# Optimization experiments

Hardware: AMD Instinct MI355X
Metric: run time of the kernel (lower is better)

## Reference

```python
import jax, jax.numpy as jnp
import numpy as np

C = 64
CQ = C // 8


def setup_inputs() -> dict:
    key = jax.random.key(0)
    ks = jax.random.split(key, 8)
    x = jax.random.normal(ks[0], (8, C, 64, 64), dtype=jnp.float32)
    s = 1.0 / np.sqrt(C)
    Wq = jax.random.normal(ks[1], (CQ, C), dtype=jnp.float32) * s
    bq = jax.random.normal(ks[2], (CQ,), dtype=jnp.float32) * s
    Wk = jax.random.normal(ks[3], (CQ, C), dtype=jnp.float32) * s
    bk = jax.random.normal(ks[4], (CQ,), dtype=jnp.float32) * s
    Wv = jax.random.normal(ks[5], (C, C), dtype=jnp.float32) * s
    bv = jax.random.normal(ks[6], (C,), dtype=jnp.float32) * s
    gamma = jnp.array([0.5], dtype=jnp.float32)  # nonzero so value path contributes
    return {"x": x, "Wq": Wq, "bq": bq, "Wk": Wk, "bk": bk, "Wv": Wv, "bv": bv, "gamma": gamma}


def reference(x, Wq, bq, Wk, bk, Wv, bv, gamma):
    B, Cc, H, W = x.shape
    xf = x.reshape(B, Cc, H * W)  # [B, C, N]
    # 1x1 conv == channel-mixing linear
    f = jnp.einsum('oc,bcn->bon', Wq, xf) + bq[None, :, None]  # [B, C/8, N]
    g = jnp.einsum('oc,bcn->bon', Wk, xf) + bk[None, :, None]  # [B, C/8, N]
    h = jnp.einsum('oc,bcn->bon', Wv, xf) + bv[None, :, None]  # [B, C, N]
    # scores[b,i,j] = f[b,:,i] . g[b,:,j]; softmax over dim=1 (query dim i)
    scores = jnp.einsum('bdi,bdj->bij', f, g)  # [B, N, N]
    beta = jax.nn.softmax(scores, axis=1)
    o = gamma[0] * jnp.einsum('bcn,bnm->bcm', h, beta) + xf
    return o.reshape(B, Cc, H, W)
```

## Files before the change

kernel.cpp:

```cpp
#include <hip/hip_runtime.h>
#include <hip/hip_fp16.h>


typedef _Float16 half8_t __attribute__((ext_vector_type(8)));
typedef _Float16 half4_t __attribute__((ext_vector_type(4)));
typedef _Float16 half2_t __attribute__((ext_vector_type(2)));
typedef __fp16  fp16x2  __attribute__((ext_vector_type(2)));
typedef float float4_t __attribute__((ext_vector_type(4)));

#define NTOK 4096
#define PRH 72
#define LOG2E 1.44269504088896340736f

#if __has_builtin(__builtin_amdgcn_exp2f)
__device__ __forceinline__ float fexp2(float x) { return __builtin_amdgcn_exp2f(x); }
#else
__device__ __forceinline__ float fexp2(float x) { return exp2f(x); }
#endif

__device__ __forceinline__ half2_t pkcvt(float a, float b) {
    fp16x2 v = __builtin_amdgcn_cvt_pkrtz(a, b);
    return __builtin_bit_cast(half2_t, v);
}

__global__ __launch_bounds__(320) void proj_kernel(
    const float* __restrict__ x,
    const float* __restrict__ Wq, const float* __restrict__ bq,
    const float* __restrict__ Wk, const float* __restrict__ bk,
    const float* __restrict__ Wv, const float* __restrict__ bv,
    __half* __restrict__ fTR, __half* __restrict__ gT16, __half* __restrict__ hM)
{
    __shared__ __align__(16) _Float16 xh[32 * PRH];
    const int t      = threadIdx.x;
    const int blk    = blockIdx.x;
    const int b      = blockIdx.y;
    const int n0     = blk * 32;
    const int kt64   = blk >> 1;
    const int t4base = (blk & 1) * 2;

    if (t < 256) {
#pragma unroll
        for (int i = 0; i < 2; i++) {
            const int idx = t + i * 256;
            const int c = idx >> 3, f4 = idx & 7;
            float4 v = *(const float4*)(x + (((size_t)(b * 64 + c)) << 12) + n0 + f4 * 4);
            const int cs = c ^ ((f4 & 3) << 4);
            xh[(f4 * 4 + 0) * PRH + cs] = (_Float16)v.x;
            xh[(f4 * 4 + 1) * PRH + cs] = (_Float16)v.y;
            xh[(f4 * 4 + 2) * PRH + cs] = (_Float16)v.z;
            xh[(f4 * 4 + 3) * PRH + cs] = (_Float16)v.w;
        }
    }

    const int w    = t >> 6;
    const int lane = t & 63;
    const int q    = lane >> 4;
    const int ml   = lane & 15;

    const float* wrow;
    if (w == 0) wrow = (ml < 8) ? (Wq + ml * 64) : (Wk + (ml - 8) * 64);
    else        wrow = Wv + ((w - 1) * 16 + ml) * 64;
    half4_t afr[4];
#pragma unroll
    for (int ks = 0; ks < 4; ks++) {
        float4 wv4 = *(const float4*)(wrow + ks * 16 + q * 4);
        afr[ks] = (half4_t){(_Float16)wv4.x, (_Float16)wv4.y,
                            (_Float16)wv4.z, (_Float16)wv4.w};
    }
    float4 bias4;
    if (w == 0) bias4 = (q < 2) ? *(const float4*)(bq + q * 4)
                                : *(const float4*)(bk + (q - 2) * 4);
    else        bias4 = *(const float4*)(bv + (w - 1) * 16 + q * 4);

    __syncthreads();

#pragma unroll
    for (int cg = 0; cg < 2; cg++) {
        const int tok  = cg * 16 + ml;
        const int swz  = (tok >> 2) & 3;
        float4_t acc = (float4_t){0.f, 0.f, 0.f, 0.f};
#pragma unroll
        for (int ks = 0; ks < 4; ks++) {
            half4_t bfr = *(const half4_t*)(&xh[tok * PRH + ((ks ^ swz) * 16 + q * 4)]);
            acc = __builtin_amdgcn_mfma_f32_16x16x16f16(afr[ks], bfr, acc, 0, 0, 0);
        }
        acc[0] += bias4.x; acc[1] += bias4.y; acc[2] += bias4.z; acc[3] += bias4.w;
        const int gtok = n0 + tok;
        const int t4   = t4base + cg;

        if (w == 0) {
            __half* rec = fTR + ((size_t)b << 16) + (size_t)(kt64 * 16 + ml) * 64;
            if (q < 2) {
                half4_t fv = {(_Float16)(acc[0] * LOG2E), (_Float16)(acc[1] * LOG2E),
                              (_Float16)(acc[2] * LOG2E), (_Float16)(acc[3] * LOG2E)};
                *(half4_t*)(rec + q * 16 + t4 * 4) = fv;
            } else {
                half4_t cv = (half4_t){};
                if (q == 2) cv[0] = (_Float16)1.0f;
                *(half4_t*)(rec + q * 16 + t4 * 4) = cv;
            }
            float gn2p = acc[0] * acc[0] + acc[1] * acc[1] +
                         acc[2] * acc[2] + acc[3] * acc[3];
            float gn2 = gn2p + __shfl_xor(gn2p, 16, 64);
            if (q >= 2) {
                half4_t gv = {(_Float16)acc[0], (_Float16)acc[1],
                              (_Float16)acc[2], (_Float16)acc[3]};
                __half* gp = gT16 + (size_t)((b << 12) + gtok) * 16;
                *(half4_t*)(gp + (q - 2) * 4) = gv;
                if (q == 2) {
                    const float M = (LOG2E * 4.6f) * __builtin_sqrtf(gn2) + 1.0f;
                    *(half4_t*)(gp + 8) = (half4_t){(_Float16)(-M), 0, 0, 0};
                } else {
                    *(half4_t*)(gp + 12) = (half4_t){};
                }
            }
        } else {
            const int ch = (w - 1) * 16 + q * 4;
#pragma unroll
            for (int r = 0; r < 4; r++)
                hM[(((size_t)b * 64 + ch + r) << 12) + gtok] = __float2half(acc[r]);
        }
    }
}

template<int NT>
__global__ __launch_bounds__(256) void attn_kernel(
    const __half* __restrict__ fTR, const __half* __restrict__ gT16,
    const __half* __restrict__ hM,
    __half* __restrict__ Pacc, float* __restrict__ Lsum)
{
    __shared__ __align__(16) _Float16 hl[2][64 * PRH];
    const int tid   = threadIdx.x;
    const int w     = tid >> 6;
    const int lane  = tid & 63;
    const int q     = lane >> 4;
    const int ml    = lane & 15;
    const int b     = blockIdx.y;
    const int split = blockIdx.z;
    const int colA  = blockIdx.x * 128 + w * 16 + ml;
    const int colB  = colA + 64;

    half4_t gfA = *(const half4_t*)(gT16 + ((size_t)((b << 12) + colA)) * 16 + q * 4);
    half4_t gfB = *(const half4_t*)(gT16 + ((size_t)((b << 12) + colB)) * 16 + q * 4);

    float4_t accA[4], accB[4];
#pragma unroll
    for (int cg = 0; cg < 4; cg++) {
        accA[cg] = (float4_t){0.f, 0.f, 0.f, 0.f};
        accB[cg] = (float4_t){0.f, 0.f, 0.f, 0.f};
    }
    float4_t accLA = (float4_t){0.f, 0.f, 0.f, 0.f};
    float4_t accLB = (float4_t){0.f, 0.f, 0.f, 0.f};
    const half4_t onesf = {(_Float16)1.0f, (_Float16)1.0f,
                           (_Float16)1.0f, (_Float16)1.0f};

    const int kt0 = split * NT;
    const int c0  = tid >> 3;
    const int g0  = tid & 7;

    const __half* srow0 = hM + ((size_t)(b * 64 + c0) << 12) + kt0 * 64 + g0 * 8;
    const __half* srow1 = srow0 + ((size_t)32 << 12);
    const __half* fptr  = fTR + ((size_t)b << 16) + (size_t)(kt0 * 16 + ml) * 64 + q * 16;

    uint4 s0 = *(const uint4*)srow0;
    uint4 s1 = *(const uint4*)srow1;
    half8_t f01 = *(const half8_t*)fptr;
    half8_t f23 = *(const half8_t*)(fptr + 8);
    *(uint4*)(&hl[0][c0 * PRH + g0 * 8])        = s0;
    *(uint4*)(&hl[0][(c0 + 32) * PRH + g0 * 8]) = s1;
    __syncthreads();

#pragma unroll 1
    for (int kt = 0; kt < NT; kt++) {
        const _Float16* hbL = &hl[kt & 1][ml * PRH + q * 4];
        half4_t afn0 = __builtin_shufflevector(f01, f01, 0, 1, 2, 3);
        half4_t afn1 = __builtin_shufflevector(f01, f01, 4, 5, 6, 7);
        half4_t afn2 = __builtin_shufflevector(f23, f23, 0, 1, 2, 3);
        half4_t afn3 = __builtin_shufflevector(f23, f23, 4, 5, 6, 7);

        float4_t stA0 = __builtin_amdgcn_mfma_f32_16x16x16f16(
            afn0, gfA, (float4_t){0.f, 0.f, 0.f, 0.f}, 0, 0, 0);
        float4_t stA1 = __builtin_amdgcn_mfma_f32_16x16x16f16(
            afn1, gfA, (float4_t){0.f, 0.f, 0.f, 0.f}, 0, 0, 0);
        float4_t stA2 = __builtin_amdgcn_mfma_f32_16x16x16f16(
            afn2, gfA, (float4_t){0.f, 0.f, 0.f, 0.f}, 0, 0, 0);
        float4_t stA3 = __builtin_amdgcn_mfma_f32_16x16x16f16(
            afn3, gfA, (float4_t){0.f, 0.f, 0.f, 0.f}, 0, 0, 0);
        float4_t stB0 = __builtin_amdgcn_mfma_f32_16x16x16f16(
            afn0, gfB, (float4_t){0.f, 0.f, 0.f, 0.f}, 0, 0, 0);
        float4_t stB1 = __builtin_amdgcn_mfma_f32_16x16x16f16(
            afn1, gfB, (float4_t){0.f, 0.f, 0.f, 0.f}, 0, 0, 0);
        float4_t stB2 = __builtin_amdgcn_mfma_f32_16x16x16f16(
            afn2, gfB, (float4_t){0.f, 0.f, 0.f, 0.f}, 0, 0, 0);
        float4_t stB3 = __builtin_amdgcn_mfma_f32_16x16x16f16(
            afn3, gfB, (float4_t){0.f, 0.f, 0.f, 0.f}, 0, 0, 0);

        if (kt + 1 < NT) {
            f01 = *(const half8_t*)(fptr + 1024);
            f23 = *(const half8_t*)(fptr + 1032);
            s0 = *(const uint4*)(srow0 + 64);
            s1 = *(const uint4*)(srow1 + 64);
            fptr  += 1024;
            srow0 += 64;
            srow1 += 64;
        }

        {
            float pA0 = fexp2(stA0[0]), pA1 = fexp2(stA0[1]),
                  pA2 = fexp2(stA0[2]), pA3 = fexp2(stA0[3]);
            float pB0 = fexp2(stB0[0]), pB1 = fexp2(stB0[1]),
                  pB2 = fexp2(stB0[2]), pB3 = fexp2(stB0[3]);
            half2_t a_lo = pkcvt(pA0, pA1), a_hi = pkcvt(pA2, pA3);
            half2_t b_lo = pkcvt(pB0, pB1), b_hi = pkcvt(pB2, pB3);
            half4_t pfA = {a_lo[0], a_lo[1], a_hi[0], a_hi[1]};
            half4_t pfB = {b_lo[0], b_lo[1], b_hi[0], b_hi[1]};
            accLA = __builtin_amdgcn_mfma_f32_16x16x16f16(onesf, pfA, accLA, 0, 0, 0);
            accLB = __builtin_amdgcn_mfma_f32_16x16x16f16(onesf, pfB, accLB, 0, 0, 0);
#pragma unroll
            for (int cg = 0; cg < 4; cg++) {
                half4_t ah = *(const half4_t*)(hbL + cg * (16 * PRH) + 0 * 16);
                accA[cg] = __builtin_amdgcn_mfma_f32_16x16x16f16(ah, pfA, accA[cg], 0, 0, 0);
                accB[cg] = __builtin_amdgcn_mfma_f32_16x16x16f16(ah, pfB, accB[cg], 0, 0, 0);
            }
        }
        {
            float pA0 = fexp2(stA1[0]), pA1 = fexp2(stA1[1]),
                  pA2 = fexp2(stA1[2]), pA3 = fexp2(stA1[3]);
            float pB0 = fexp2(stB1[0]), pB1 = fexp2(stB1[1]),
                  pB2 = fexp2(stB1[2]), pB3 = fexp2(stB1[3]);
            half2_t a_lo = pkcvt(pA0, pA1), a_hi = pkcvt(pA2, pA3);
            half2_t b_lo = pkcvt(pB0, pB1), b_hi = pkcvt(pB2, pB3);
            half4_t pfA = {a_lo[0], a_lo[1], a_hi[0], a_hi[1]};
            half4_t pfB = {b_lo[0], b_lo[1], b_hi[0], b_hi[1]};
            accLA = __builtin_amdgcn_mfma_f32_16x16x16f16(onesf, pfA, accLA, 0, 0, 0);
            accLB = __builtin_amdgcn_mfma_f32_16x16x16f16(onesf, pfB, accLB, 0, 0, 0);
#pragma unroll
            for (int cg = 0; cg < 4; cg++) {
                half4_t ah = *(const half4_t*)(hbL + cg * (16 * PRH) + 1 * 16);
                accA[cg] = __builtin_amdgcn_mfma_f32_16x16x16f16(ah, pfA, accA[cg], 0, 0, 0);
                accB[cg] = __builtin_amdgcn_mfma_f32_16x16x16f16(ah, pfB, accB[cg], 0, 0, 0);
            }
        }
        {
            float pA0 = fexp2(stA2[0]), pA1 = fexp2(stA2[1]),
                  pA2 = fexp2(stA2[2]), pA3 = fexp2(stA2[3]);
            float pB0 = fexp2(stB2[0]), pB1 = fexp2(stB2[1]),
                  pB2 = fexp2(stB2[2]), pB3 = fexp2(stB2[3]);
            half2_t a_lo = pkcvt(pA0, pA1), a_hi = pkcvt(pA2, pA3);
            half2_t b_lo = pkcvt(pB0, pB1), b_hi = pkcvt(pB2, pB3);
            half4_t pfA = {a_lo[0], a_lo[1], a_hi[0], a_hi[1]};
            half4_t pfB = {b_lo[0], b_lo[1], b_hi[0], b_hi[1]};
            accLA = __builtin_amdgcn_mfma_f32_16x16x16f16(onesf, pfA, accLA, 0, 0, 0);
            accLB = __builtin_amdgcn_mfma_f32_16x16x16f16(onesf, pfB, accLB, 0, 0, 0);
#pragma unroll
            for (int cg = 0; cg < 4; cg++) {
                half4_t ah = *(const half4_t*)(hbL + cg * (16 * PRH) + 2 * 16);
                accA[cg] = __builtin_amdgcn_mfma_f32_16x16x16f16(ah, pfA, accA[cg], 0, 0, 0);
                accB[cg] = __builtin_amdgcn_mfma_f32_16x16x16f16(ah, pfB, accB[cg], 0, 0, 0);
            }
        }
        {
            float pA0 = fexp2(stA3[0]), pA1 = fexp2(stA3[1]),
                  pA2 = fexp2(stA3[2]), pA3 = fexp2(stA3[3]);
            float pB0 = fexp2(stB3[0]), pB1 = fexp2(stB3[1]),
                  pB2 = fexp2(stB3[2]), pB3 = fexp2(stB3[3]);
            half2_t a_lo = pkcvt(pA0, pA1), a_hi = pkcvt(pA2, pA3);
            half2_t b_lo = pkcvt(pB0, pB1), b_hi = pkcvt(pB2, pB3);
            half4_t pfA = {a_lo[0], a_lo[1], a_hi[0], a_hi[1]};
            half4_t pfB = {b_lo[0], b_lo[1], b_hi[0], b_hi[1]};
            accLA = __builtin_amdgcn_mfma_f32_16x16x16f16(onesf, pfA, accLA, 0, 0, 0);
            accLB = __builtin_amdgcn_mfma_f32_16x16x16f16(onesf, pfB, accLB, 0, 0, 0);
#pragma unroll
            for (int cg = 0; cg < 4; cg++) {
                half4_t ah = *(const half4_t*)(hbL + cg * (16 * PRH) + 3 * 16);
                accA[cg] = __builtin_amdgcn_mfma_f32_16x16x16f16(ah, pfA, accA[cg], 0, 0, 0);
                accB[cg] = __builtin_amdgcn_mfma_f32_16x16x16f16(ah, pfB, accB[cg], 0, 0, 0);
            }
        }

        if (kt + 1 < NT) {
            _Float16* hn = &hl[(kt + 1) & 1][0];
            *(uint4*)(&hn[c0 * PRH + g0 * 8])        = s0;
            *(uint4*)(&hn[(c0 + 32) * PRH + g0 * 8]) = s1;
        }
        __syncthreads();
    }

    __half* pa = Pacc + (((size_t)(split * 8 + b) * 64) << 12);
#pragma unroll
    for (int cg = 0; cg < 4; cg++)
#pragma unroll
        for (int r = 0; r < 4; r++) {
            int ch = cg * 16 + q * 4 + r;
            pa[((size_t)ch << 12) + colA] = __float2half(accA[cg][r]);
            pa[((size_t)ch << 12) + colB] = __float2half(accB[cg][r]);
        }
    if (q == 0) {
        Lsum[((size_t)(split * 8 + b) << 12) + colA] = accLA[0];
        Lsum[((size_t)(split * 8 + b) << 12) + colB] = accLB[0];
    }
}

template<int S>
__global__ __launch_bounds__(256) void merge_kernel(
    const __half* __restrict__ Pacc, const float* __restrict__ Lsum,
    const float* __restrict__ x, const float* __restrict__ gammap,
    float* __restrict__ out)
{
    __shared__ float invL[64];
    const int tid  = threadIdx.x;
    const int c4   = tid & 15;
    const int chh  = tid >> 4;
    const int b    = blockIdx.y;
    const int col0 = blockIdx.x * 64;
    const int ch   = blockIdx.z * 16 + chh;

    if (tid < 64) {
        float L = 0.f;
#pragma unroll
        for (int s = 0; s < S; s++)
            L += Lsum[((size_t)(s * 8 + b) << 12) + col0 + tid];
        invL[tid] = gammap[0] / L;
    }
    __syncthreads();

    const int cc = c4 * 4;
    const size_t base = (((size_t)b * 64 + ch) << 12) + col0 + cc;
    float4 xv = *(const float4*)(x + base);
    float o0 = 0.f, o1 = 0.f, o2 = 0.f, o3 = 0.f;
#pragma unroll
    for (int s = 0; s < S; s++) {
        half4_t pv = *(const half4_t*)(Pacc +
            (((size_t)(s * 8 + b) * 64 + ch) << 12) + col0 + cc);
        o0 += (float)pv[0];
        o1 += (float)pv[1];
        o2 += (float)pv[2];
        o3 += (float)pv[3];
    }
    float4 ov;
    ov.x = o0 * invL[cc]     + xv.x;
    ov.y = o1 * invL[cc + 1] + xv.y;
    ov.z = o2 * invL[cc + 2] + xv.z;
    ov.w = o3 * invL[cc + 3] + xv.w;
    *(float4*)(out + base) = ov;
}

extern "C" void kernel_launch(void* const* d_in, const int* in_sizes, int n_in,
                              void* d_out, int out_size, void* d_ws, size_t ws_size,
                              hipStream_t stream) {
    const float* x     = (const float*)d_in[0];
    const float* Wq    = (const float*)d_in[1];
    const float* bq    = (const float*)d_in[2];
    const float* Wk    = (const float*)d_in[3];
    const float* bk    = (const float*)d_in[4];
    const float* Wv    = (const float*)d_in[5];
    const float* bv    = (const float*)d_in[6];
    const float* gamma = (const float*)d_in[7];
    float* out = (float*)d_out;

    const size_t fr_bytes  = (size_t)8 * 65536 * 2;
    const size_t g_bytes   = (size_t)8 * NTOK * 16 * 2;
    const size_t hM_bytes  = (size_t)8 * 64 * NTOK * 2;
    const size_t pa_split  = (size_t)8 * 64 * NTOK * 2;
    const size_t l_split   = (size_t)8 * NTOK * sizeof(float);
    const size_t base_need = fr_bytes + g_bytes + hM_bytes;

    int S = 1;
    if (ws_size >= base_need + 4 * (pa_split + l_split)) S = 4;
    else if (ws_size >= base_need + 2 * (pa_split + l_split)) S = 2;

    char* p = (char*)d_ws;
    __half* fTR  = (__half*)p;  p += fr_bytes;
    __half* gT16 = (__half*)p;  p += g_bytes;
    __half* hM   = (__half*)p;  p += hM_bytes;
    __half* Pacc = (__half*)p;  p += (size_t)S * pa_split;
    float*  Lsum = (float*)p;

    proj_kernel<<<dim3(128, 8), 320, 0, stream>>>(x, Wq, bq, Wk, bk, Wv, bv,
                                                  fTR, gT16, hM);
    if (S == 4) {
        attn_kernel<16><<<dim3(32, 8, 4), 256, 0, stream>>>(fTR, gT16, hM, Pacc, Lsum);
        merge_kernel<4><<<dim3(64, 8, 4), 256, 0, stream>>>(Pacc, Lsum, x, gamma, out);
    } else if (S == 2) {
        attn_kernel<32><<<dim3(32, 8, 2), 256, 0, stream>>>(fTR, gT16, hM, Pacc, Lsum);
        merge_kernel<2><<<dim3(64, 8, 4), 256, 0, stream>>>(Pacc, Lsum, x, gamma, out);
    } else {
        attn_kernel<64><<<dim3(32, 8, 1), 256, 0, stream>>>(fTR, gT16, hM, Pacc, Lsum);
        merge_kernel<1><<<dim3(64, 8, 4), 256, 0, stream>>>(Pacc, Lsum, x, gamma, out);
    }
}
```

Baseline: 122.7 us.

## Use 16x16x32 MFMA for PV, add setprio, and allow 8-way key split

Merges pairs of key sub-blocks so the probability-times-value products and row-sum accumulations use the K=32 MFMA instruction, halving the number of MFMA issues in the inner loop. It also raises wave priority around the MFMA blocks with s_setprio. It adds an 8-way split over the key dimension when workspace allows, giving 2048 blocks instead of 1024 to fill the CUs better. The cost is a larger partial buffer and more work in the merge kernel. The new split also depends on how big the workspace is.

Measured after the change: 123.0 us. About the same (+0.2%).

```diff
diff --git a/kernel.cpp b/kernel.cpp
--- a/kernel.cpp
+++ b/kernel.cpp
@@ -123,6 +123,39 @@
     }
 }
 
+#define PAIR(SEA, SOA, SEB, SOB, OFF)                                           \
+    {                                                                           \
+        float eA0 = fexp2(SEA[0]), eA1 = fexp2(SEA[1]),                         \
+              eA2 = fexp2(SEA[2]), eA3 = fexp2(SEA[3]);                         \
+        float oA0 = fexp2(SOA[0]), oA1 = fexp2(SOA[1]),                         \
+              oA2 = fexp2(SOA[2]), oA3 = fexp2(SOA[3]);                         \
+        float eB0 = fexp2(SEB[0]), eB1 = fexp2(SEB[1]),                         \
+              eB2 = fexp2(SEB[2]), eB3 = fexp2(SEB[3]);                         \
+        float oB0 = fexp2(SOB[0]), oB1 = fexp2(SOB[1]),                         \
+              oB2 = fexp2(SOB[2]), oB3 = fexp2(SOB[3]);                         \
+        half2_t eaA = pkcvt(eA0, eA1), ebA = pkcvt(eA2, eA3);                   \
+        half2_t oaA = pkcvt(oA0, oA1), obA = pkcvt(oA2, oA3);                   \
+        half2_t eaB = pkcvt(eB0, eB1), ebB = pkcvt(eB2, eB3);                   \
+        half2_t oaB = pkcvt(oB0, oB1), obB = pkcvt(oB2, oB3);                   \
+        half8_t pA8 = {eaA[0], eaA[1], ebA[0], ebA[1],                          \
+                       oaA[0], oaA[1], obA[0], obA[1]};                         \
+        half8_t pB8 = {eaB[0], eaB[1], ebB[0], ebB[1],                          \
+                       oaB[0], oaB[1], obB[0], obB[1]};                         \
+        __builtin_amdgcn_s_setprio(1);                                          \
+        accLA = __builtin_amdgcn_mfma_f32_16x16x32_f16(ones8, pA8, accLA, 0, 0, 0); \
+        accLB = __builtin_amdgcn_mfma_f32_16x16x32_f16(ones8, pB8, accLB, 0, 0, 0); \
+        _Pragma("unroll")                                                       \
+        for (int cg = 0; cg < 4; cg++) {                                        \
+            half4_t ahE = *(const half4_t*)(hbL + cg * (16 * PRH) + (OFF));     \
+            half4_t ahO = *(const half4_t*)(hbL + cg * (16 * PRH) + (OFF) + 16);\
+            half8_t ah8 = {ahE[0], ahE[1], ahE[2], ahE[3],                      \
+                           ahO[0], ahO[1], ahO[2], ahO[3]};                     \
+            accA[cg] = __builtin_amdgcn_mfma_f32_16x16x32_f16(ah8, pA8, accA[cg], 0, 0, 0); \
+            accB[cg] = __builtin_amdgcn_mfma_f32_16x16x32_f16(ah8, pB8, accB[cg], 0, 0, 0); \
+        }                                                                       \
+        __builtin_amdgcn_s_setprio(0);                                          \
+    }
+
 template<int NT>
 __global__ __launch_bounds__(256) void attn_kernel(
     const __half* __restrict__ fTR, const __half* __restrict__ gT16,
@@ -151,7 +184,8 @@
     }
     float4_t accLA = (float4_t){0.f, 0.f, 0.f, 0.f};
     float4_t accLB = (float4_t){0.f, 0.f, 0.f, 0.f};
-    const half4_t onesf = {(_Float16)1.0f, (_Float16)1.0f,
+    const half8_t ones8 = {(_Float16)1.0f, (_Float16)1.0f, (_Float16)1.0f,
+                           (_Float16)1.0f, (_Float16)1.0f, (_Float16)1.0f,
                            (_Float16)1.0f, (_Float16)1.0f};
 
     const int kt0 = split * NT;
@@ -178,6 +212,7 @@
         half4_t afn2 = __builtin_shufflevector(f23, f23, 0, 1, 2, 3);
         half4_t afn3 = __builtin_shufflevector(f23, f23, 4, 5, 6, 7);
 
+        __builtin_amdgcn_s_setprio(1);
         float4_t stA0 = __builtin_amdgcn_mfma_f32_16x16x16f16(
             afn0, gfA, (float4_t){0.f, 0.f, 0.f, 0.f}, 0, 0, 0);
         float4_t stA1 = __builtin_amdgcn_mfma_f32_16x16x16f16(
@@ -194,6 +229,7 @@
             afn2, gfB, (float4_t){0.f, 0.f, 0.f, 0.f}, 0, 0, 0);
         float4_t stB3 = __builtin_amdgcn_mfma_f32_16x16x16f16(
             afn3, gfB, (float4_t){0.f, 0.f, 0.f, 0.f}, 0, 0, 0);
+        __builtin_amdgcn_s_setprio(0);
 
         if (kt + 1 < NT) {
             f01 = *(const half8_t*)(fptr + 1024);
@@ -205,78 +241,8 @@
             srow1 += 64;
         }
 
-        {
-            float pA0 = fexp2(stA0[0]), pA1 = fexp2(stA0[1]),
-                  pA2 = fexp2(stA0[2]), pA3 = fexp2(stA0[3]);
-            float pB0 = fexp2(stB0[0]), pB1 = fexp2(stB0[1]),
-                  pB2 = fexp2(stB0[2]), pB3 = fexp2(stB0[3]);
-            half2_t a_lo = pkcvt(pA0, pA1), a_hi = pkcvt(pA2, pA3);
-            half2_t b_lo = pkcvt(pB0, pB1), b_hi = pkcvt(pB2, pB3);
-            half4_t pfA = {a_lo[0], a_lo[1], a_hi[0], a_hi[1]};
-            half4_t pfB = {b_lo[0], b_lo[1], b_hi[0], b_hi[1]};
-            accLA = __builtin_amdgcn_mfma_f32_16x16x16f16(onesf, pfA, accLA, 0, 0, 0);
-            accLB = __builtin_amdgcn_mfma_f32_16x16x16f16(onesf, pfB, accLB, 0, 0, 0);
-#pragma unroll
-            for (int cg = 0; cg < 4; cg++) {
-                half4_t ah = *(const half4_t*)(hbL + cg * (16 * PRH) + 0 * 16);
-                accA[cg] = __builtin_amdgcn_mfma_f32_16x16x16f16(ah, pfA, accA[cg], 0, 0, 0);
-                accB[cg] = __builtin_amdgcn_mfma_f32_16x16x16f16(ah, pfB, accB[cg], 0, 0, 0);
-            }
-        }
-        {
-            float pA0 = fexp2(stA1[0]), pA1 = fexp2(stA1[1]),
-                  pA2 = fexp2(stA1[2]), pA3 = fexp2(stA1[3]);
-            float pB0 = fexp2(stB1[0]), pB1 = fexp2(stB1[1]),
-                  pB2 = fexp2(stB1[2]), pB3 = fexp2(stB1[3]);
-            half2_t a_lo = pkcvt(pA0, pA1), a_hi = pkcvt(pA2, pA3);
-            half2_t b_lo = pkcvt(pB0, pB1), b_hi = pkcvt(pB2, pB3);
-            half4_t pfA = {a_lo[0], a_lo[1], a_hi[0], a_hi[1]};
-            half4_t pfB = {b_lo[0], b_lo[1], b_hi[0], b_hi[1]};
-            accLA = __builtin_amdgcn_mfma_f32_16x16x16f16(onesf, pfA, accLA, 0, 0, 0);
-            accLB = __builtin_amdgcn_mfma_f32_16x16x16f16(onesf, pfB, accLB, 0, 0, 0);
-#pragma unroll
-            for (int cg = 0; cg < 4; cg++) {
-                half4_t ah = *(const half4_t*)(hbL + cg * (16 * PRH) + 1 * 16);
-                accA[cg] = __builtin_amdgcn_mfma_f32_16x16x16f16(ah, pfA, accA[cg], 0, 0, 0);
-                accB[cg] = __builtin_amdgcn_mfma_f32_16x16x16f16(ah, pfB, accB[cg], 0, 0, 0);
-            }
-        }
-        {
-            float pA0 = fexp2(stA2[0]), pA1 = fexp2(stA2[1]),
-                  pA2 = fexp2(stA2[2]), pA3 = fexp2(stA2[3]);
-            float pB0 = fexp2(stB2[0]), pB1 = fexp2(stB2[1]),
-                  pB2 = fexp2(stB2[2]), pB3 = fexp2(stB2[3]);
-            half2_t a_lo = pkcvt(pA0, pA1), a_hi = pkcvt(pA2, pA3);
-            half2_t b_lo = pkcvt(pB0, pB1), b_hi = pkcvt(pB2, pB3);
-            half4_t pfA = {a_lo[0], a_lo[1], a_hi[0], a_hi[1]};
-            half4_t pfB = {b_lo[0], b_lo[1], b_hi[0], b_hi[1]};
-            accLA = __builtin_amdgcn_mfma_f32_16x16x16f16(onesf, pfA, accLA, 0, 0, 0);
-            accLB = __builtin_amdgcn_mfma_f32_16x16x16f16(onesf, pfB, accLB, 0, 0, 0);
-#pragma unroll
-            for (int cg = 0; cg < 4; cg++) {
-                half4_t ah = *(const half4_t*)(hbL + cg * (16 * PRH) + 2 * 16);
-                accA[cg] = __builtin_amdgcn_mfma_f32_16x16x16f16(ah, pfA, accA[cg], 0, 0, 0);
-                accB[cg] = __builtin_amdgcn_mfma_f32_16x16x16f16(ah, pfB, accB[cg], 0, 0, 0);
-            }
-        }
-        {
-            float pA0 = fexp2(stA3[0]), pA1 = fexp2(stA3[1]),
-                  pA2 = fexp2(stA3[2]), pA3 = fexp2(stA3[3]);
-            float pB0 = fexp2(stB3[0]), pB1 = fexp2(stB3[1]),
-                  pB2 = fexp2(stB3[2]), pB3 = fexp2(stB3[3]);
-            half2_t a_lo = pkcvt(pA0, pA1), a_hi = pkcvt(pA2, pA3);
-            half2_t b_lo = pkcvt(pB0, pB1), b_hi = pkcvt(pB2, pB3);
-            half4_t pfA = {a_lo[0], a_lo[1], a_hi[0], a_hi[1]};
-            half4_t pfB = {b_lo[0], b_lo[1], b_hi[0], b_hi[1]};
-            accLA = __builtin_amdgcn_mfma_f32_16x16x16f16(onesf, pfA, accLA, 0, 0, 0);
-            accLB = __builtin_amdgcn_mfma_f32_16x16x16f16(onesf, pfB, accLB, 0, 0, 0);
-#pragma unroll
-            for (int cg = 0; cg < 4; cg++) {
-                half4_t ah = *(const half4_t*)(hbL + cg * (16 * PRH) + 3 * 16);
-                accA[cg] = __builtin_amdgcn_mfma_f32_16x16x16f16(ah, pfA, accA[cg], 0, 0, 0);
-                accB[cg] = __builtin_amdgcn_mfma_f32_16x16x16f16(ah, pfB, accB[cg], 0, 0, 0);
-            }
-        }
+        PAIR(stA0, stA1, stB0, stB1, 0)
+        PAIR(stA2, stA3, stB2, stB3, 32)
 
         if (kt + 1 < NT) {
             _Float16* hn = &hl[(kt + 1) & 1][0];
@@ -366,7 +332,8 @@
     const size_t base_need = fr_bytes + g_bytes + hM_bytes;
 
     int S = 1;
-    if (ws_size >= base_need + 4 * (pa_split + l_split)) S = 4;
+    if (ws_size >= base_need + 8 * (pa_split + l_split)) S = 8;
+    else if (ws_size >= base_need + 4 * (pa_split + l_split)) S = 4;
     else if (ws_size >= base_need + 2 * (pa_split + l_split)) S = 2;
 
     char* p = (char*)d_ws;
@@ -378,7 +345,10 @@
 
     proj_kernel<<<dim3(128, 8), 320, 0, stream>>>(x, Wq, bq, Wk, bk, Wv, bv,
                                                   fTR, gT16, hM);
-    if (S == 4) {
+    if (S == 8) {
+        attn_kernel<8><<<dim3(32, 8, 8), 256, 0, stream>>>(fTR, gT16, hM, Pacc, Lsum);
+        merge_kernel<8><<<dim3(64, 8, 4), 256, 0, stream>>>(Pacc, Lsum, x, gamma, out);
+    } else if (S == 4) {
         attn_kernel<16><<<dim3(32, 8, 4), 256, 0, stream>>>(fTR, gT16, hM, Pacc, Lsum);
         merge_kernel<4><<<dim3(64, 8, 4), 256, 0, stream>>>(Pacc, Lsum, x, gamma, out);
     } else if (S == 2) {
```
